# Kernel optimization log

Measured on AMD Instinct MI355X. Metric: run time of the kernel, lower is better.

Reference implementation:

```python
import jax, jax.numpy as jnp
import numpy as np

B, T, D, H, L = 64, 512, 1024, 1024, 2


def _make_params(key, in_size, hidden):
    # 4 input-to-hidden and 4 hidden-to-hidden matrices, gate order (i, f, n, o),
    # concatenated along the output axis -> one GEMM per source per step.
    k1, k2 = jax.random.split(key)
    sx = (6.0 / (in_size + hidden)) ** 0.5   # xavier_uniform bound
    sh = (6.0 / (hidden + hidden)) ** 0.5
    Wx = jax.random.uniform(k1, (in_size, 4 * hidden), minval=-sx, maxval=sx, dtype=jnp.float32)
    Wh = jax.random.uniform(k2, (hidden, 4 * hidden), minval=-sh, maxval=sh, dtype=jnp.float32)
    b = jnp.zeros((4 * hidden,), dtype=jnp.float32)
    return Wx, Wh, b


def setup_inputs() -> dict:
    key = jax.random.key(0)
    kx, k0, k1 = jax.random.split(key, 3)
    x = jax.random.normal(kx, (B, T, D), dtype=jnp.float32)
    h0 = jnp.zeros((L, B, H), dtype=jnp.float32)
    c0 = jnp.zeros((L, B, H), dtype=jnp.float32)
    Wx0, Wh0, b0 = _make_params(k0, D, H)
    Wx1, Wh1, b1 = _make_params(k1, H, H)
    return {"x": x, "h0": h0, "c0": c0,
            "Wx0": Wx0, "Wh0": Wh0, "b0": b0,
            "Wx1": Wx1, "Wh1": Wh1, "b1": b1}


def _run_layer(xseq, h, c, Wx, Wh, b):
    # xseq: [T, B, in], h/c: [B, H]
    def step(carry, xt):
        h, c = carry
        g = xt @ Wx + h @ Wh + b                       # [B, 4H]
        i_t, f_t, n_t, o_t = jnp.split(g, 4, axis=-1)
        i_t = jax.nn.sigmoid(i_t)
        f_t = jax.nn.sigmoid(f_t)
        n_t = jnp.tanh(n_t)
        o_t = jax.nn.sigmoid(o_t)
        c = f_t * c + i_t * n_t
        h = o_t * jnp.tanh(c)
        return (h, c), h
    (h, c), ys = jax.lax.scan(step, (h, c), xseq)
    return ys, h, c                                     # ys: [T, B, H]


def reference(x, h0, c0, Wx0, Wh0, b0, Wx1, Wh1, b1):
    xs = jnp.transpose(x, (1, 0, 2))                    # [T, B, D]
    params = [(Wx0, Wh0, b0), (Wx1, Wh1, b1)]
    hs, cs = [], []
    for layer in range(L):
        Wx, Wh, b = params[layer]
        xs, h, c = _run_layer(xs, h0[layer], c0[layer], Wx, Wh, b)
        hs.append(h)
        cs.append(c)
    outputs = jnp.transpose(xs, (1, 0, 2))              # [B, T, H]
    return outputs, (jnp.stack(hs, 0), jnp.stack(cs, 0))
```

## Files before the change

### kernel.cpp

```cpp
#include <hip/hip_runtime.h>


#define NBLK 256
#define TPB  512
#define T_   512
#define HS_OFF 33554432
#define CS_OFF 33685504

typedef float  f32x4  __attribute__((ext_vector_type(4)));
typedef short  bf16x8 __attribute__((ext_vector_type(8)));

#define WS_CTR  0u
#define WS_W    69632u
#define WS_BIAS 33624064u
#define WS_XB   33656832u
#define WS_H0   100765696u
#define WS_H1   101027840u
#define WS_MIN  101289984u
#define WS_XG   101289984u
#define WS_BIG  369725440u

__device__ __forceinline__ unsigned short f2bf(float f) {
  union { float f; unsigned u; } v; v.f = f;
  return (unsigned short)((v.u + 0x7FFFu + ((v.u >> 16) & 1u)) >> 16);
}
__device__ __forceinline__ float bf2f(unsigned short s) {
  union { unsigned u; float f; } v; v.u = ((unsigned)s) << 16;
  return v.f;
}
__device__ __forceinline__ float fsig(float x) { return 1.0f / (1.0f + __expf(-x)); }
__device__ __forceinline__ float ftanh(float x) {
  x = fminf(15.0f, fmaxf(-15.0f, x));
  float e = __expf(2.0f * x);
  return (e - 1.0f) / (e + 1.0f);
}

__global__ void kw(const float* __restrict__ Wx0, const float* __restrict__ Wh0,
                   const float* __restrict__ Wx1, const float* __restrict__ Wh1,
                   unsigned short* __restrict__ wp) {
  __shared__ float tile[64][65];
  int tb = blockIdx.x;
  int m  = tb >> 10;
  int kt = (tb >> 6) & 15;
  int nt = tb & 63;
  const float* W = (m == 0) ? Wx0 : (m == 1) ? Wh0 : (m == 2) ? Wx1 : Wh1;
  unsigned short* O = wp + (size_t)m * 4194304u;
  int k0 = kt * 64, n0 = nt * 64;
  int tx = threadIdx.x & 63, tg = threadIdx.x >> 6;
  for (int r = tg; r < 64; r += 4)
    tile[r][tx] = W[(size_t)(k0 + r) * 4096 + n0 + tx];
  __syncthreads();
  for (int r = tg; r < 64; r += 4) {
    int n = n0 + r;
    int p = ((n & 1023) << 2) | (n >> 10);
    O[(size_t)p * 1024 + k0 + tx] = f2bf(tile[tx][r]);
  }
}

__global__ void kx(const float* __restrict__ x, unsigned short* __restrict__ xb) {
  int row = blockIdx.x;
  int t = row >> 6, b = row & 63;
  const float4* src = (const float4*)(x + ((size_t)b * 512 + t) * 1024);
  float4 f = src[threadIdx.x];
  ushort4 o; o.x = f2bf(f.x); o.y = f2bf(f.y); o.z = f2bf(f.z); o.w = f2bf(f.w);
  ((ushort4*)(xb + (size_t)row * 1024))[threadIdx.x] = o;
}

__global__ void kmisc(const float* __restrict__ b0, const float* __restrict__ b1,
                      const float* __restrict__ h0in,
                      float* __restrict__ biasP,
                      unsigned short* __restrict__ h0r, unsigned short* __restrict__ h1r) {
  int idx = blockIdx.x * 256 + threadIdx.x;
  if (idx < 8192) {
    int layer = idx >> 12, p = idx & 4095;
    int orig = (p & 3) * 1024 + (p >> 2);
    biasP[idx] = (layer ? b1 : b0)[orig];
  } else if (idx < 139264) {
    int e = idx - 8192;
    int layer = e >> 16, o = e & 65535;
    int row = o >> 10, col = o & 1023;
    unsigned short v = f2bf(h0in[layer * 65536 + o]);
    int dst = 65536 + (col >> 3) * 512 + row * 8 + (col & 7);
    if (layer) h1r[dst] = v; else h0r[dst] = v;
  }
}

__global__ void __launch_bounds__(512, 2)
kxg(const unsigned short* __restrict__ wp, const unsigned short* __restrict__ xb,
    unsigned short* __restrict__ xg) {
  __shared__ char sm[73728];
  float* red = (float*)(sm + 65536);
  const int tid = threadIdx.x;
  const int w = tid >> 6, l = tid & 63;
  const int cb = blockIdx.x >> 4;
  const int tc = blockIdx.x & 15;
  const int rt = w & 3, kh = w >> 2;

  const char* src = (const char*)(wp + (size_t)(cb * 32) * 1024u);
  for (int i = tid; i < 4096; i += 512) {
    int sb = i << 4;
    int c  = sb >> 11;
    int kb = sb & 2047;
    *(uint4*)(sm + (c << 11) + (kb ^ ((c & 7) << 4))) = *(const uint4*)(src + sb);
  }
  __syncthreads();

  const int ae0 = (rt * 16 + (l & 15)) * 1024 + kh * 512 + (l >> 4) * 8;
  const int kb2 = kh * 1024 + (l >> 4) * 16;
  const int swz = (l & 7) << 4;
  const int lb0 = (l & 15) << 11;
  const int lb1 = ((l & 15) + 16) << 11;

  for (int t = tc * 32; t < tc * 32 + 32; ++t) {
    const unsigned short* xt = xb + (size_t)t * 65536u;
    f32x4 a0 = {0.f, 0.f, 0.f, 0.f};
    f32x4 a1 = {0.f, 0.f, 0.f, 0.f};
    #pragma unroll
    for (int kk = 0; kk < 16; ++kk) {
      bf16x8 ax = *(const bf16x8*)(xt + ae0 + kk * 32);
      const int kb = (kb2 + kk * 64) ^ swz;
      bf16x8 b0 = *(const bf16x8*)(sm + lb0 + kb);
      bf16x8 b1 = *(const bf16x8*)(sm + lb1 + kb);
      a0 = __builtin_amdgcn_mfma_f32_16x16x32_bf16(ax, b0, a0, 0, 0, 0);
      a1 = __builtin_amdgcn_mfma_f32_16x16x32_bf16(ax, b1, a1, 0, 0, 0);
    }
    if (kh == 1) {
      float* r0 = red + (size_t)((rt * 2 + 0) * 64 + l) * 4;
      float* r1 = red + (size_t)((rt * 2 + 1) * 64 + l) * 4;
      #pragma unroll
      for (int v = 0; v < 4; ++v) { r0[v] = a0[v]; r1[v] = a1[v]; }
    }
    __syncthreads();
    if (kh == 0) {
      const float* r0 = red + (size_t)((rt * 2 + 0) * 64 + l) * 4;
      const float* r1 = red + (size_t)((rt * 2 + 1) * 64 + l) * 4;
      ushort4 o0, o1;
      o0.x = f2bf(a0[0] + r0[0]); o0.y = f2bf(a0[1] + r0[1]);
      o0.z = f2bf(a0[2] + r0[2]); o0.w = f2bf(a0[3] + r0[3]);
      o1.x = f2bf(a1[0] + r1[0]); o1.y = f2bf(a1[1] + r1[1]);
      o1.z = f2bf(a1[2] + r1[2]); o1.w = f2bf(a1[3] + r1[3]);
      *(ushort4*)(xg + ((((size_t)t * 256 + (cb * 2 + 0)) * 4 + rt) * 64 + l) * 4) = o0;
      *(ushort4*)(xg + ((((size_t)t * 256 + (cb * 2 + 1)) * 4 + rt) * 64 + l) * 4) = o1;
    }
    __syncthreads();
  }
}

__global__ void __launch_bounds__(TPB)
klstm(const float* __restrict__ c0_in,
      const unsigned short* __restrict__ wp,
      const float* __restrict__ biasP,
      const unsigned short* __restrict__ xb,
      const unsigned short* __restrict__ xg,
      unsigned short* __restrict__ h0ring,
      unsigned short* __restrict__ h1ring,
      unsigned* __restrict__ ctrbase,
      float* __restrict__ out,
      int use_xg) {
  extern __shared__ char smem[];
  float* red = (float*)(smem + 131072);
  float* lhb = (float*)(smem + 139264);
  unsigned* gctr  = ctrbase;
  unsigned* rctr  = ctrbase + 8192;
  unsigned* gflag = ctrbase + 9216;
  const int tid = threadIdx.x;
  const int w   = tid >> 6;
  const int l   = tid & 63;
  const int bid = blockIdx.x;
  const int n0  = bid * 16;
  const int layer = w >> 2;
  const int rbase = (w & 3) * 16;
  const int khalf = (w >> 2) * 512;
  const int grp   = bid >> 5;
  float* lh = lhb + w * 64;

  for (int m = 0; m < 4; m += 2) {
    const char* src = (const char*)(wp + (size_t)m * 4194304u + (size_t)n0 * 1024u);
    char* dst = smem + m * 32768;
    for (int i = tid; i < 2048; i += TPB) {
      int sb = i << 4;
      int c  = sb >> 11;
      int kb = sb & 2047;
      *(uint4*)(dst + (c << 11) + (kb ^ ((c & 7) << 4))) = *(const uint4*)(src + sb);
    }
  }

  bf16x8 wh0f[16], wh1f[16];
  {
    const unsigned short* p0 = wp + 4194304u + (size_t)(n0 + (l & 15)) * 1024u + khalf + (l >> 4) * 8;
    const unsigned short* p1 = wp + 3u * 4194304u + (size_t)(n0 + (l & 15)) * 1024u + khalf + (l >> 4) * 8;
    #pragma unroll
    for (int ks = 0; ks < 16; ++ks) {
      wh0f[ks] = *(const bf16x8*)(p0 + ks * 32);
      wh1f[ks] = *(const bf16x8*)(p1 + ks * 32);
    }
  }

  const int jg = bid * 4 + ((l & 15) >> 2);
  const float biasv = biasP[layer * 4096 + n0 + (l & 15)];
  const int qb = l & ~3;

  float cr[4];
  #pragma unroll
  for (int v = 0; v < 4; ++v)
    cr[v] = c0_in[layer * 65536 + (rbase + (l >> 4) * 4 + v) * 1024 + jg];
  __syncthreads();

  const int ae0  = (rbase + (l & 15)) * 1024 + khalf + (l >> 4) * 8;
  const int hbase = ((khalf >> 3) + (l >> 4)) * 512 + (rbase + (l & 15)) * 8;
  const int lb0  = (l & 15) << 11;
  const int kb2  = khalf * 2 + (l >> 4) * 16;
  const int swz  = (l & 7) << 4;
  const int hsto = (bid >> 1) * 512 + 4 * (bid & 1);

  float xgf[4] = {0.f, 0.f, 0.f, 0.f};
  if (use_xg && w < 4) {
    ushort4 xv = *(const ushort4*)(xg + (((size_t)bid * 4 + w) * 64 + l) * 4);
    xgf[0] = bf2f(xv.x); xgf[1] = bf2f(xv.y); xgf[2] = bf2f(xv.z); xgf[3] = bf2f(xv.w);
  }

  for (int k = 0; k <= T_; ++k) {
    #pragma unroll
    for (int ks = 0; ks < 16; ++ks) {
      asm volatile("" :: "v"(wh0f[ks]));
      asm volatile("" :: "v"(wh1f[ks]));
    }

    const unsigned short* h0p = h0ring + ((k + 1) & 1) * 65536;
    const unsigned short* h1p = h1ring + (k & 1) * 65536;

    f32x4 acc0  = {0.f, 0.f, 0.f, 0.f};
    f32x4 acc0b = {0.f, 0.f, 0.f, 0.f};
    f32x4 acc1a = {0.f, 0.f, 0.f, 0.f};
    f32x4 acc1b = {0.f, 0.f, 0.f, 0.f};
    if (use_xg) {
      #pragma unroll
      for (int kk = 0; kk < 16; ++kk) {
        bf16x8 ah0 = *(const bf16x8*)(h0p + hbase + kk * 2048);
        bf16x8 ah1 = *(const bf16x8*)(h1p + hbase + kk * 2048);
        const int bo = lb0 + ((kb2 + kk * 64) ^ swz);
        bf16x8 bx1 = *(const bf16x8*)(smem + 65536 + bo);
        acc0  = __builtin_amdgcn_mfma_f32_16x16x32_bf16(ah0, wh0f[kk], acc0, 0, 0, 0);
        acc1a = __builtin_amdgcn_mfma_f32_16x16x32_bf16(ah0, bx1, acc1a, 0, 0, 0);
        acc1b = __builtin_amdgcn_mfma_f32_16x16x32_bf16(ah1, wh1f[kk], acc1b, 0, 0, 0);
      }
    } else {
      const unsigned short* xt = xb + (size_t)((k < T_) ? k : (T_ - 1)) * 65536u;
      #pragma unroll
      for (int kk = 0; kk < 16; ++kk) {
        bf16x8 ax  = *(const bf16x8*)(xt + ae0 + kk * 32);
        bf16x8 ah0 = *(const bf16x8*)(h0p + hbase + kk * 2048);
        bf16x8 ah1 = *(const bf16x8*)(h1p + hbase + kk * 2048);
        const int bo = lb0 + ((kb2 + kk * 64) ^ swz);
        bf16x8 bx0 = *(const bf16x8*)(smem + bo);
        bf16x8 bx1 = *(const bf16x8*)(smem + 65536 + bo);
        acc0b = __builtin_amdgcn_mfma_f32_16x16x32_bf16(ax,  bx0, acc0b, 0, 0, 0);
        acc0  = __builtin_amdgcn_mfma_f32_16x16x32_bf16(ah0, wh0f[kk], acc0, 0, 0, 0);
        acc1a = __builtin_amdgcn_mfma_f32_16x16x32_bf16(ah0, bx1, acc1a, 0, 0, 0);
        acc1b = __builtin_amdgcn_mfma_f32_16x16x32_bf16(ah1, wh1f[kk], acc1b, 0, 0, 0);
      }
    }

    {
      float* rb = red + (size_t)(w * 64 + l) * 4;
      f32x4 other = layer ? (acc0 + acc0b) : (acc1a + acc1b);
      #pragma unroll
      for (int v = 0; v < 4; ++v) rb[v] = other[v];
    }
    __syncthreads();

    f32x4 g = layer ? (acc1a + acc1b) : (acc0 + acc0b);
    {
      const int pw = layer ? (w - 4) : (w + 4);
      const float* rb = red + (size_t)(pw * 64 + l) * 4;
      #pragma unroll
      for (int v = 0; v < 4; ++v) g[v] += rb[v];
    }
    if (use_xg && w < 4) {
      #pragma unroll
      for (int v = 0; v < 4; ++v) g[v] += xgf[v];
    }

    const bool active = layer ? (k >= 1) : (k < T_);
    f32x4 outv = {0.f, 0.f, 0.f, 0.f};
    if (active) {
      unsigned short* hw = layer ? (h1ring + ((k + 1) & 1) * 65536)
                                 : (h0ring + (k & 1) * 65536);
      #pragma unroll
      for (int v = 0; v < 4; ++v) {
        float gv = g[v] + biasv;
        float gi = __shfl(gv, qb);
        float gf = __shfl(gv, qb | 1);
        float gn = __shfl(gv, qb | 2);
        float go = __shfl(gv, qb | 3);
        float i_ = fsig(gi), f_ = fsig(gf), n_ = ftanh(gn), o_ = fsig(go);
        float c = f_ * cr[v] + i_ * n_;
        cr[v] = c;
        float h = o_ * ftanh(c);
        if ((l & 3) == 0)
          lh[((l >> 4) * 4 + v) * 4 + ((l & 15) >> 2)] = h;
      }
      if (l < 16) {
        f32x4 h4 = *(f32x4*)(lh + l * 4);
        outv = h4;
        ushort4 u4;
        u4.x = f2bf(h4[0]); u4.y = f2bf(h4[1]); u4.z = f2bf(h4[2]); u4.w = f2bf(h4[3]);
        union { ushort4 s; unsigned long long q; } pk; pk.s = u4;
        __hip_atomic_store((unsigned long long*)(hw + hsto + (rbase + l) * 8), pk.q,
                           __ATOMIC_RELAXED, __HIP_MEMORY_SCOPE_AGENT);
      }
    }

    if (k < T_) {
      __syncthreads();
      if (tid == 0) {
        unsigned old = __hip_atomic_fetch_add(&gctr[grp * 1024 + k], 1u,
                                              __ATOMIC_RELAXED, __HIP_MEMORY_SCOPE_AGENT);
        if (old == 31u) {
          unsigned oldr = __hip_atomic_fetch_add(&rctr[k], 1u,
                                                 __ATOMIC_RELAXED, __HIP_MEMORY_SCOPE_AGENT);
          if (oldr == 7u) {
            #pragma unroll
            for (int gg = 0; gg < 8; ++gg)
              __hip_atomic_store(&gflag[gg * 1024 + k], 1u,
                                 __ATOMIC_RELAXED, __HIP_MEMORY_SCOPE_AGENT);
          }
        }
        __builtin_amdgcn_fence(__ATOMIC_ACQUIRE, "agent");
      }
    }

    if (active && l < 16) {
      const int row = rbase + l;
      if (layer) {
        *(f32x4*)(out + (size_t)row * 524288u + (size_t)(k - 1) * 1024u + bid * 4) = outv;
        if (k == T_)
          *(f32x4*)(out + HS_OFF + 65536 + row * 1024 + bid * 4) = outv;
      } else if (k == T_ - 1) {
        *(f32x4*)(out + HS_OFF + row * 1024 + bid * 4) = outv;
      }
    }
    if (use_xg && w < 4 && k + 1 < T_) {
      ushort4 xv = *(const ushort4*)(xg + ((((size_t)(k + 1) * 256 + bid) * 4 + w) * 64 + l) * 4);
      xgf[0] = bf2f(xv.x); xgf[1] = bf2f(xv.y); xgf[2] = bf2f(xv.z); xgf[3] = bf2f(xv.w);
    }

    if (k < T_) {
      if (tid == 0) {
        unsigned spins = 0;
        while (__hip_atomic_load(&gflag[grp * 1024 + k], __ATOMIC_RELAXED, __HIP_MEMORY_SCOPE_AGENT) == 0u) {
          __builtin_amdgcn_s_sleep(1);
          if (++spins > 67108864u) break;
        }
      }
      __syncthreads();
    }
  }

  if ((l & 3) == 0) {
    #pragma unroll
    for (int v = 0; v < 4; ++v)
      out[CS_OFF + layer * 65536 + (rbase + (l >> 4) * 4 + v) * 1024 + jg] = cr[v];
  }
}

extern "C" void kernel_launch(void* const* d_in, const int* in_sizes, int n_in,
                              void* d_out, int out_size, void* d_ws, size_t ws_size,
                              hipStream_t stream) {
  const float* x   = (const float*)d_in[0];
  const float* h0  = (const float*)d_in[1];
  const float* c0  = (const float*)d_in[2];
  const float* Wx0 = (const float*)d_in[3];
  const float* Wh0 = (const float*)d_in[4];
  const float* b0  = (const float*)d_in[5];
  const float* Wx1 = (const float*)d_in[6];
  const float* Wh1 = (const float*)d_in[7];
  const float* b1  = (const float*)d_in[8];
  float* out = (float*)d_out;
  char* ws = (char*)d_ws;
  if (ws_size < (size_t)WS_MIN) return;
  const int use_xg = (ws_size >= (size_t)WS_BIG) ? 1 : 0;

  unsigned* ctr       = (unsigned*)(ws + WS_CTR);
  unsigned short* wp  = (unsigned short*)(ws + WS_W);
  float* biasP        = (float*)(ws + WS_BIAS);
  unsigned short* xbp = (unsigned short*)(ws + WS_XB);
  unsigned short* h0r = (unsigned short*)(ws + WS_H0);
  unsigned short* h1r = (unsigned short*)(ws + WS_H1);
  unsigned short* xgp = (unsigned short*)(ws + WS_XG);

  (void)hipMemsetAsync(ctr, 0, 69632, stream);
  hipLaunchKernelGGL(kw,    dim3(4096),  dim3(256), 0, stream, Wx0, Wh0, Wx1, Wh1, wp);
  hipLaunchKernelGGL(kx,    dim3(32768), dim3(256), 0, stream, x, xbp);
  hipLaunchKernelGGL(kmisc, dim3(544),   dim3(256), 0, stream, b0, b1, h0, biasP, h0r, h1r);
  if (use_xg)
    hipLaunchKernelGGL(kxg, dim3(2048),  dim3(512), 0, stream, wp, xbp, xgp);

  (void)hipFuncSetAttribute((const void*)klstm, hipFuncAttributeMaxDynamicSharedMemorySize, 141312);
  const float* c0a = c0; const unsigned short* wpa = wp; const float* bpa = biasP;
  const unsigned short* xba = xbp; const unsigned short* xga = xgp;
  unsigned short* h0a = h0r; unsigned short* h1a = h1r;
  unsigned* ca = ctr; float* oa = out; int uxg = use_xg;
  void* args[] = {&c0a, &wpa, &bpa, &xba, &xga, &h0a, &h1a, &ca, &oa, &uxg};
  hipError_t e = hipLaunchCooperativeKernel((const void*)klstm, dim3(NBLK), dim3(TPB),
                                            args, 141312, stream);
  if (e != hipSuccess) {
    hipLaunchKernelGGL(klstm, dim3(NBLK), dim3(TPB), 141312, stream,
                       c0a, wpa, bpa, xba, xga, h0a, h1a, ca, oa, uxg);
  }
}
```

Baseline: 5.768 ms.

## Double threads per block and split K across wave pairs per layer

```diff
diff --git a/kernel.cpp b/kernel.cpp
--- a/kernel.cpp
+++ b/kernel.cpp
@@ -2,7 +2,7 @@
 
 
 #define NBLK 256
-#define TPB  512
+#define TPB  1024
 #define T_   512
 #define HS_OFF 33554432
 #define CS_OFF 33685504
@@ -158,8 +158,8 @@
       float* __restrict__ out,
       int use_xg) {
   extern __shared__ char smem[];
-  float* red = (float*)(smem + 131072);
-  float* lhb = (float*)(smem + 139264);
+  float* red = (float*)(smem + 65536);
+  float* lhb = (float*)(smem + 73728);
   unsigned* gctr  = ctrbase;
   unsigned* rctr  = ctrbase + 8192;
   unsigned* gflag = ctrbase + 9216;
@@ -168,42 +168,52 @@
   const int l   = tid & 63;
   const int bid = blockIdx.x;
   const int n0  = bid * 16;
-  const int layer = w >> 2;
-  const int rbase = (w & 3) * 16;
-  const int khalf = (w >> 2) * 512;
+  const int lay = w >> 3;
+  const int rt  = (w >> 1) & 3;
+  const int kh  = w & 1;
+  const int rbase = rt * 16;
+  const int khalf = kh * 512;
   const int grp   = bid >> 5;
-  float* lh = lhb + w * 64;
-
-  for (int m = 0; m < 4; m += 2) {
-    const char* src = (const char*)(wp + (size_t)m * 4194304u + (size_t)n0 * 1024u);
-    char* dst = smem + m * 32768;
+  const int slot  = lay * 4 + rt;
+  float* lh = lhb + slot * 64;
+
+  {
+    const char* src = (const char*)(wp + 2u * 4194304u + (size_t)n0 * 1024u);
     for (int i = tid; i < 2048; i += TPB) {
       int sb = i << 4;
       int c  = sb >> 11;
       int kb = sb & 2047;
-      *(uint4*)(dst + (c << 11) + (kb ^ ((c & 7) << 4))) = *(const uint4*)(src + sb);
-    }
-  }
-
-  bf16x8 wh0f[16], wh1f[16];
+      *(uint4*)(smem + (c << 11) + (kb ^ ((c & 7) << 4))) = *(const uint4*)(src + sb);
+    }
+    if (!use_xg) {
+      const char* s0 = (const char*)(wp + (size_t)n0 * 1024u);
+      for (int i = tid; i < 2048; i += TPB) {
+        int sb = i << 4;
+        int c  = sb >> 11;
+        int kb = sb & 2047;
+        *(uint4*)(smem + 32768 + (c << 11) + (kb ^ ((c & 7) << 4))) = *(const uint4*)(s0 + sb);
+      }
+    }
+  }
+
+  bf16x8 whf[16];
   {
-    const unsigned short* p0 = wp + 4194304u + (size_t)(n0 + (l & 15)) * 1024u + khalf + (l >> 4) * 8;
-    const unsigned short* p1 = wp + 3u * 4194304u + (size_t)(n0 + (l & 15)) * 1024u + khalf + (l >> 4) * 8;
+    const unsigned short* pw_ = wp + (size_t)(lay ? 3u : 1u) * 4194304u
+                              + (size_t)(n0 + (l & 15)) * 1024u + khalf + (l >> 4) * 8;
     #pragma unroll
-    for (int ks = 0; ks < 16; ++ks) {
-      wh0f[ks] = *(const bf16x8*)(p0 + ks * 32);
-      wh1f[ks] = *(const bf16x8*)(p1 + ks * 32);
-    }
+    for (int ks = 0; ks < 16; ++ks) whf[ks] = *(const bf16x8*)(pw_ + ks * 32);
   }
 
   const int jg = bid * 4 + ((l & 15) >> 2);
-  const float biasv = biasP[layer * 4096 + n0 + (l & 15)];
+  const float biasv = biasP[lay * 4096 + n0 + (l & 15)];
   const int qb = l & ~3;
 
-  float cr[4];
-  #pragma unroll
-  for (int v = 0; v < 4; ++v)
-    cr[v] = c0_in[layer * 65536 + (rbase + (l >> 4) * 4 + v) * 1024 + jg];
+  float cr[4] = {0.f, 0.f, 0.f, 0.f};
+  if (kh == 0) {
+    #pragma unroll
+    for (int v = 0; v < 4; ++v)
+      cr[v] = c0_in[lay * 65536 + (rbase + (l >> 4) * 4 + v) * 1024 + jg];
+  }
   __syncthreads();
 
   const int ae0  = (rbase + (l & 15)) * 1024 + khalf + (l >> 4) * 8;
@@ -214,78 +224,69 @@
   const int hsto = (bid >> 1) * 512 + 4 * (bid & 1);
 
   float xgf[4] = {0.f, 0.f, 0.f, 0.f};
-  if (use_xg && w < 4) {
-    ushort4 xv = *(const ushort4*)(xg + (((size_t)bid * 4 + w) * 64 + l) * 4);
+  if (use_xg && lay == 0 && kh == 0) {
+    ushort4 xv = *(const ushort4*)(xg + (((size_t)bid * 4 + rt) * 64 + l) * 4);
     xgf[0] = bf2f(xv.x); xgf[1] = bf2f(xv.y); xgf[2] = bf2f(xv.z); xgf[3] = bf2f(xv.w);
   }
 
   for (int k = 0; k <= T_; ++k) {
     #pragma unroll
-    for (int ks = 0; ks < 16; ++ks) {
-      asm volatile("" :: "v"(wh0f[ks]));
-      asm volatile("" :: "v"(wh1f[ks]));
-    }
+    for (int ks = 0; ks < 16; ++ks) asm volatile("" :: "v"(whf[ks]));
 
     const unsigned short* h0p = h0ring + ((k + 1) & 1) * 65536;
     const unsigned short* h1p = h1ring + (k & 1) * 65536;
 
-    f32x4 acc0  = {0.f, 0.f, 0.f, 0.f};
-    f32x4 acc0b = {0.f, 0.f, 0.f, 0.f};
-    f32x4 acc1a = {0.f, 0.f, 0.f, 0.f};
-    f32x4 acc1b = {0.f, 0.f, 0.f, 0.f};
-    if (use_xg) {
+    f32x4 accA = {0.f, 0.f, 0.f, 0.f};
+    f32x4 accB = {0.f, 0.f, 0.f, 0.f};
+    if (lay == 0) {
+      #pragma unroll
+      for (int kk = 0; kk < 16; ++kk) {
+        bf16x8 ah0 = *(const bf16x8*)(h0p + hbase + kk * 2048);
+        accA = __builtin_amdgcn_mfma_f32_16x16x32_bf16(ah0, whf[kk], accA, 0, 0, 0);
+      }
+      if (!use_xg) {
+        const unsigned short* xt = xb + (size_t)((k < T_) ? k : (T_ - 1)) * 65536u;
+        #pragma unroll
+        for (int kk = 0; kk < 16; ++kk) {
+          bf16x8 ax  = *(const bf16x8*)(xt + ae0 + kk * 32);
+          bf16x8 bx0 = *(const bf16x8*)(smem + 32768 + lb0 + ((kb2 + kk * 64) ^ swz));
+          accB = __builtin_amdgcn_mfma_f32_16x16x32_bf16(ax, bx0, accB, 0, 0, 0);
+        }
+      }
+    } else {
       #pragma unroll
       for (int kk = 0; kk < 16; ++kk) {
         bf16x8 ah0 = *(const bf16x8*)(h0p + hbase + kk * 2048);
         bf16x8 ah1 = *(const bf16x8*)(h1p + hbase + kk * 2048);
-        const int bo = lb0 + ((kb2 + kk * 64) ^ swz);
-        bf16x8 bx1 = *(const bf16x8*)(smem + 65536 + bo);
-        acc0  = __builtin_amdgcn_mfma_f32_16x16x32_bf16(ah0, wh0f[kk], acc0, 0, 0, 0);
-        acc1a = __builtin_amdgcn_mfma_f32_16x16x32_bf16(ah0, bx1, acc1a, 0, 0, 0);
-        acc1b = __builtin_amdgcn_mfma_f32_16x16x32_bf16(ah1, wh1f[kk], acc1b, 0, 0, 0);
-      }
-    } else {
-      const unsigned short* xt = xb + (size_t)((k < T_) ? k : (T_ - 1)) * 65536u;
+        bf16x8 bx1 = *(const bf16x8*)(smem + lb0 + ((kb2 + kk * 64) ^ swz));
+        accA = __builtin_amdgcn_mfma_f32_16x16x32_bf16(ah0, bx1, accA, 0, 0, 0);
+        accB = __builtin_amdgcn_mfma_f32_16x16x32_bf16(ah1, whf[kk], accB, 0, 0, 0);
+      }
+    }
+
+    if (kh == 1) {
+      float* rb = red + (size_t)slot * 256 + (size_t)l * 4;
+      f32x4 s = accA + accB;
       #pragma unroll
-      for (int kk = 0; kk < 16; ++kk) {
-        bf16x8 ax  = *(const bf16x8*)(xt + ae0 + kk * 32);
-        bf16x8 ah0 = *(const bf16x8*)(h0p + hbase + kk * 2048);
-        bf16x8 ah1 = *(const bf16x8*)(h1p + hbase + kk * 2048);
-        const int bo = lb0 + ((kb2 + kk * 64) ^ swz);
-        bf16x8 bx0 = *(const bf16x8*)(smem + bo);
-        bf16x8 bx1 = *(const bf16x8*)(smem + 65536 + bo);
-        acc0b = __builtin_amdgcn_mfma_f32_16x16x32_bf16(ax,  bx0, acc0b, 0, 0, 0);
-        acc0  = __builtin_amdgcn_mfma_f32_16x16x32_bf16(ah0, wh0f[kk], acc0, 0, 0, 0);
-        acc1a = __builtin_amdgcn_mfma_f32_16x16x32_bf16(ah0, bx1, acc1a, 0, 0, 0);
-        acc1b = __builtin_amdgcn_mfma_f32_16x16x32_bf16(ah1, wh1f[kk], acc1b, 0, 0, 0);
-      }
-    }
-
-    {
-      float* rb = red + (size_t)(w * 64 + l) * 4;
-      f32x4 other = layer ? (acc0 + acc0b) : (acc1a + acc1b);
-      #pragma unroll
-      for (int v = 0; v < 4; ++v) rb[v] = other[v];
+      for (int v = 0; v < 4; ++v) rb[v] = s[v];
     }
     __syncthreads();
 
-    f32x4 g = layer ? (acc1a + acc1b) : (acc0 + acc0b);
-    {
-      const int pw = layer ? (w - 4) : (w + 4);
-      const float* rb = red + (size_t)(pw * 64 + l) * 4;
-      #pragma unroll
-      for (int v = 0; v < 4; ++v) g[v] += rb[v];
-    }
-    if (use_xg && w < 4) {
-      #pragma unroll
-      for (int v = 0; v < 4; ++v) g[v] += xgf[v];
-    }
-
-    const bool active = layer ? (k >= 1) : (k < T_);
+    const bool active = lay ? (k >= 1) : (k < T_);
     f32x4 outv = {0.f, 0.f, 0.f, 0.f};
-    if (active) {
-      unsigned short* hw = layer ? (h1ring + ((k + 1) & 1) * 65536)
-                                 : (h0ring + (k & 1) * 65536);
+    if (kh == 0 && active) {
+      f32x4 g = accA + accB;
+      {
+        const float* rb = red + (size_t)slot * 256 + (size_t)l * 4;
+        #pragma unroll
+        for (int v = 0; v < 4; ++v) g[v] += rb[v];
+      }
+      if (lay == 0) {
+        #pragma unroll
+        for (int v = 0; v < 4; ++v) g[v] += xgf[v];
+      }
+      unsigned short* hw = lay ? (h1ring + ((k + 1) & 1) * 65536)
+                               : (h0ring + (k & 1) * 65536);
       #pragma unroll
       for (int v = 0; v < 4; ++v) {
         float gv = g[v] + biasv;
@@ -330,9 +331,9 @@
       }
     }
 
-    if (active && l < 16) {
+    if (kh == 0 && active && l < 16) {
       const int row = rbase + l;
-      if (layer) {
+      if (lay) {
         *(f32x4*)(out + (size_t)row * 524288u + (size_t)(k - 1) * 1024u + bid * 4) = outv;
         if (k == T_)
           *(f32x4*)(out + HS_OFF + 65536 + row * 1024 + bid * 4) = outv;
@@ -340,8 +341,8 @@
         *(f32x4*)(out + HS_OFF + row * 1024 + bid * 4) = outv;
       }
     }
-    if (use_xg && w < 4 && k + 1 < T_) {
-      ushort4 xv = *(const ushort4*)(xg + ((((size_t)(k + 1) * 256 + bid) * 4 + w) * 64 + l) * 4);
+    if (use_xg && lay == 0 && kh == 0 && k + 1 < T_) {
+      ushort4 xv = *(const ushort4*)(xg + ((((size_t)(k + 1) * 256 + bid) * 4 + rt) * 64 + l) * 4);
       xgf[0] = bf2f(xv.x); xgf[1] = bf2f(xv.y); xgf[2] = bf2f(xv.z); xgf[3] = bf2f(xv.w);
     }
 
@@ -357,10 +358,10 @@
     }
   }
 
-  if ((l & 3) == 0) {
+  if (kh == 0 && (l & 3) == 0) {
     #pragma unroll
     for (int v = 0; v < 4; ++v)
-      out[CS_OFF + layer * 65536 + (rbase + (l >> 4) * 4 + v) * 1024 + jg] = cr[v];
+      out[CS_OFF + lay * 65536 + (rbase + (l >> 4) * 4 + v) * 1024 + jg] = cr[v];
   }
 }
 
@@ -396,16 +397,16 @@
   if (use_xg)
     hipLaunchKernelGGL(kxg, dim3(2048),  dim3(512), 0, stream, wp, xbp, xgp);
 
-  (void)hipFuncSetAttribute((const void*)klstm, hipFuncAttributeMaxDynamicSharedMemorySize, 141312);
+  (void)hipFuncSetAttribute((const void*)klstm, hipFuncAttributeMaxDynamicSharedMemorySize, 75776);
   const float* c0a = c0; const unsigned short* wpa = wp; const float* bpa = biasP;
   const unsigned short* xba = xbp; const unsigned short* xga = xgp;
   unsigned short* h0a = h0r; unsigned short* h1a = h1r;
   unsigned* ca = ctr; float* oa = out; int uxg = use_xg;
   void* args[] = {&c0a, &wpa, &bpa, &xba, &xga, &h0a, &h1a, &ca, &oa, &uxg};
   hipError_t e = hipLaunchCooperativeKernel((const void*)klstm, dim3(NBLK), dim3(TPB),
-                                            args, 141312, stream);
+                                            args, 75776, stream);
   if (e != hipSuccess) {
-    hipLaunchKernelGGL(klstm, dim3(NBLK), dim3(TPB), 141312, stream,
+    hipLaunchKernelGGL(klstm, dim3(NBLK), dim3(TPB), 75776, stream,
                        c0a, wpa, bpa, xba, xga, h0a, h1a, ca, oa, uxg);
   }
 }
```

Result: slower. 6.571 ms (+13.9%).

## Drop precomputed x-projection kernel; compute next-step layer-0 input GEMM inside recurrent loop

Applied to the files above, without the earlier changes.

```diff
diff --git a/kernel.cpp b/kernel.cpp
--- a/kernel.cpp
+++ b/kernel.cpp
@@ -17,16 +17,10 @@
 #define WS_H0   100765696u
 #define WS_H1   101027840u
 #define WS_MIN  101289984u
-#define WS_XG   101289984u
-#define WS_BIG  369725440u
 
 __device__ __forceinline__ unsigned short f2bf(float f) {
   union { float f; unsigned u; } v; v.f = f;
   return (unsigned short)((v.u + 0x7FFFu + ((v.u >> 16) & 1u)) >> 16);
-}
-__device__ __forceinline__ float bf2f(unsigned short s) {
-  union { unsigned u; float f; } v; v.u = ((unsigned)s) << 16;
-  return v.f;
 }
 __device__ __forceinline__ float fsig(float x) { return 1.0f / (1.0f + __expf(-x)); }
 __device__ __forceinline__ float ftanh(float x) {
@@ -85,81 +79,19 @@
   }
 }
 
-__global__ void __launch_bounds__(512, 2)
-kxg(const unsigned short* __restrict__ wp, const unsigned short* __restrict__ xb,
-    unsigned short* __restrict__ xg) {
-  __shared__ char sm[73728];
-  float* red = (float*)(sm + 65536);
-  const int tid = threadIdx.x;
-  const int w = tid >> 6, l = tid & 63;
-  const int cb = blockIdx.x >> 4;
-  const int tc = blockIdx.x & 15;
-  const int rt = w & 3, kh = w >> 2;
-
-  const char* src = (const char*)(wp + (size_t)(cb * 32) * 1024u);
-  for (int i = tid; i < 4096; i += 512) {
-    int sb = i << 4;
-    int c  = sb >> 11;
-    int kb = sb & 2047;
-    *(uint4*)(sm + (c << 11) + (kb ^ ((c & 7) << 4))) = *(const uint4*)(src + sb);
-  }
-  __syncthreads();
-
-  const int ae0 = (rt * 16 + (l & 15)) * 1024 + kh * 512 + (l >> 4) * 8;
-  const int kb2 = kh * 1024 + (l >> 4) * 16;
-  const int swz = (l & 7) << 4;
-  const int lb0 = (l & 15) << 11;
-  const int lb1 = ((l & 15) + 16) << 11;
-
-  for (int t = tc * 32; t < tc * 32 + 32; ++t) {
-    const unsigned short* xt = xb + (size_t)t * 65536u;
-    f32x4 a0 = {0.f, 0.f, 0.f, 0.f};
-    f32x4 a1 = {0.f, 0.f, 0.f, 0.f};
-    #pragma unroll
-    for (int kk = 0; kk < 16; ++kk) {
-      bf16x8 ax = *(const bf16x8*)(xt + ae0 + kk * 32);
-      const int kb = (kb2 + kk * 64) ^ swz;
-      bf16x8 b0 = *(const bf16x8*)(sm + lb0 + kb);
-      bf16x8 b1 = *(const bf16x8*)(sm + lb1 + kb);
-      a0 = __builtin_amdgcn_mfma_f32_16x16x32_bf16(ax, b0, a0, 0, 0, 0);
-      a1 = __builtin_amdgcn_mfma_f32_16x16x32_bf16(ax, b1, a1, 0, 0, 0);
-    }
-    if (kh == 1) {
-      float* r0 = red + (size_t)((rt * 2 + 0) * 64 + l) * 4;
-      float* r1 = red + (size_t)((rt * 2 + 1) * 64 + l) * 4;
-      #pragma unroll
-      for (int v = 0; v < 4; ++v) { r0[v] = a0[v]; r1[v] = a1[v]; }
-    }
-    __syncthreads();
-    if (kh == 0) {
-      const float* r0 = red + (size_t)((rt * 2 + 0) * 64 + l) * 4;
-      const float* r1 = red + (size_t)((rt * 2 + 1) * 64 + l) * 4;
-      ushort4 o0, o1;
-      o0.x = f2bf(a0[0] + r0[0]); o0.y = f2bf(a0[1] + r0[1]);
-      o0.z = f2bf(a0[2] + r0[2]); o0.w = f2bf(a0[3] + r0[3]);
-      o1.x = f2bf(a1[0] + r1[0]); o1.y = f2bf(a1[1] + r1[1]);
-      o1.z = f2bf(a1[2] + r1[2]); o1.w = f2bf(a1[3] + r1[3]);
-      *(ushort4*)(xg + ((((size_t)t * 256 + (cb * 2 + 0)) * 4 + rt) * 64 + l) * 4) = o0;
-      *(ushort4*)(xg + ((((size_t)t * 256 + (cb * 2 + 1)) * 4 + rt) * 64 + l) * 4) = o1;
-    }
-    __syncthreads();
-  }
-}
-
 __global__ void __launch_bounds__(TPB)
 klstm(const float* __restrict__ c0_in,
       const unsigned short* __restrict__ wp,
       const float* __restrict__ biasP,
       const unsigned short* __restrict__ xb,
-      const unsigned short* __restrict__ xg,
       unsigned short* __restrict__ h0ring,
       unsigned short* __restrict__ h1ring,
       unsigned* __restrict__ ctrbase,
-      float* __restrict__ out,
-      int use_xg) {
+      float* __restrict__ out) {
   extern __shared__ char smem[];
-  float* red = (float*)(smem + 131072);
-  float* lhb = (float*)(smem + 139264);
+  float* red  = (float*)(smem + 65536);
+  float* lhb  = (float*)(smem + 73728);
+  float* xred = (float*)(smem + 75776);
   unsigned* gctr  = ctrbase;
   unsigned* rctr  = ctrbase + 8192;
   unsigned* gflag = ctrbase + 9216;
@@ -176,7 +108,7 @@
 
   for (int m = 0; m < 4; m += 2) {
     const char* src = (const char*)(wp + (size_t)m * 4194304u + (size_t)n0 * 1024u);
-    char* dst = smem + m * 32768;
+    char* dst = smem + (m >> 1) * 32768;
     for (int i = tid; i < 2048; i += TPB) {
       int sb = i << 4;
       int c  = sb >> 11;
@@ -204,7 +136,6 @@
   #pragma unroll
   for (int v = 0; v < 4; ++v)
     cr[v] = c0_in[layer * 65536 + (rbase + (l >> 4) * 4 + v) * 1024 + jg];
-  __syncthreads();
 
   const int ae0  = (rbase + (l & 15)) * 1024 + khalf + (l >> 4) * 8;
   const int hbase = ((khalf >> 3) + (l >> 4)) * 512 + (rbase + (l & 15)) * 8;
@@ -213,11 +144,23 @@
   const int swz  = (l & 7) << 4;
   const int hsto = (bid >> 1) * 512 + 4 * (bid & 1);
 
-  float xgf[4] = {0.f, 0.f, 0.f, 0.f};
-  if (use_xg && w < 4) {
-    ushort4 xv = *(const ushort4*)(xg + (((size_t)bid * 4 + w) * 64 + l) * 4);
-    xgf[0] = bf2f(xv.x); xgf[1] = bf2f(xv.y); xgf[2] = bf2f(xv.z); xgf[3] = bf2f(xv.w);
-  }
+  __syncthreads();
+
+  f32x4 xacc = {0.f, 0.f, 0.f, 0.f};
+  {
+    #pragma unroll
+    for (int kk = 0; kk < 16; ++kk) {
+      bf16x8 ax = *(const bf16x8*)(xb + ae0 + kk * 32);
+      bf16x8 b  = *(const bf16x8*)(smem + lb0 + ((kb2 + kk * 64) ^ swz));
+      xacc = __builtin_amdgcn_mfma_f32_16x16x32_bf16(ax, b, xacc, 0, 0, 0);
+    }
+    if (w >= 4) {
+      float* xr = xred + (size_t)(w & 3) * 256 + (size_t)l * 4;
+      #pragma unroll
+      for (int v = 0; v < 4; ++v) xr[v] = xacc[v];
+    }
+  }
+  __syncthreads();
 
   for (int k = 0; k <= T_; ++k) {
     #pragma unroll
@@ -230,55 +173,37 @@
     const unsigned short* h1p = h1ring + (k & 1) * 65536;
 
     f32x4 acc0  = {0.f, 0.f, 0.f, 0.f};
-    f32x4 acc0b = {0.f, 0.f, 0.f, 0.f};
     f32x4 acc1a = {0.f, 0.f, 0.f, 0.f};
     f32x4 acc1b = {0.f, 0.f, 0.f, 0.f};
-    if (use_xg) {
-      #pragma unroll
-      for (int kk = 0; kk < 16; ++kk) {
-        bf16x8 ah0 = *(const bf16x8*)(h0p + hbase + kk * 2048);
-        bf16x8 ah1 = *(const bf16x8*)(h1p + hbase + kk * 2048);
-        const int bo = lb0 + ((kb2 + kk * 64) ^ swz);
-        bf16x8 bx1 = *(const bf16x8*)(smem + 65536 + bo);
-        acc0  = __builtin_amdgcn_mfma_f32_16x16x32_bf16(ah0, wh0f[kk], acc0, 0, 0, 0);
-        acc1a = __builtin_amdgcn_mfma_f32_16x16x32_bf16(ah0, bx1, acc1a, 0, 0, 0);
-        acc1b = __builtin_amdgcn_mfma_f32_16x16x32_bf16(ah1, wh1f[kk], acc1b, 0, 0, 0);
-      }
-    } else {
-      const unsigned short* xt = xb + (size_t)((k < T_) ? k : (T_ - 1)) * 65536u;
-      #pragma unroll
-      for (int kk = 0; kk < 16; ++kk) {
-        bf16x8 ax  = *(const bf16x8*)(xt + ae0 + kk * 32);
-        bf16x8 ah0 = *(const bf16x8*)(h0p + hbase + kk * 2048);
-        bf16x8 ah1 = *(const bf16x8*)(h1p + hbase + kk * 2048);
-        const int bo = lb0 + ((kb2 + kk * 64) ^ swz);
-        bf16x8 bx0 = *(const bf16x8*)(smem + bo);
-        bf16x8 bx1 = *(const bf16x8*)(smem + 65536 + bo);
-        acc0b = __builtin_amdgcn_mfma_f32_16x16x32_bf16(ax,  bx0, acc0b, 0, 0, 0);
-        acc0  = __builtin_amdgcn_mfma_f32_16x16x32_bf16(ah0, wh0f[kk], acc0, 0, 0, 0);
-        acc1a = __builtin_amdgcn_mfma_f32_16x16x32_bf16(ah0, bx1, acc1a, 0, 0, 0);
-        acc1b = __builtin_amdgcn_mfma_f32_16x16x32_bf16(ah1, wh1f[kk], acc1b, 0, 0, 0);
-      }
+    #pragma unroll
+    for (int kk = 0; kk < 16; ++kk) {
+      bf16x8 ah0 = *(const bf16x8*)(h0p + hbase + kk * 2048);
+      bf16x8 ah1 = *(const bf16x8*)(h1p + hbase + kk * 2048);
+      bf16x8 bx1 = *(const bf16x8*)(smem + 32768 + lb0 + ((kb2 + kk * 64) ^ swz));
+      acc0  = __builtin_amdgcn_mfma_f32_16x16x32_bf16(ah0, wh0f[kk], acc0, 0, 0, 0);
+      acc1a = __builtin_amdgcn_mfma_f32_16x16x32_bf16(ah0, bx1, acc1a, 0, 0, 0);
+      acc1b = __builtin_amdgcn_mfma_f32_16x16x32_bf16(ah1, wh1f[kk], acc1b, 0, 0, 0);
     }
 
     {
       float* rb = red + (size_t)(w * 64 + l) * 4;
-      f32x4 other = layer ? (acc0 + acc0b) : (acc1a + acc1b);
+      f32x4 other = layer ? acc0 : (acc1a + acc1b);
       #pragma unroll
       for (int v = 0; v < 4; ++v) rb[v] = other[v];
     }
     __syncthreads();
 
-    f32x4 g = layer ? (acc1a + acc1b) : (acc0 + acc0b);
+    f32x4 g = layer ? (acc1a + acc1b) : acc0;
     {
       const int pw = layer ? (w - 4) : (w + 4);
       const float* rb = red + (size_t)(pw * 64 + l) * 4;
       #pragma unroll
       for (int v = 0; v < 4; ++v) g[v] += rb[v];
     }
-    if (use_xg && w < 4) {
-      #pragma unroll
-      for (int v = 0; v < 4; ++v) g[v] += xgf[v];
+    if (w < 4) {
+      const float* xr = xred + (size_t)w * 256 + (size_t)l * 4;
+      #pragma unroll
+      for (int v = 0; v < 4; ++v) g[v] += xacc[v] + xr[v];
     }
 
     const bool active = layer ? (k >= 1) : (k < T_);
@@ -340,9 +265,22 @@
         *(f32x4*)(out + HS_OFF + row * 1024 + bid * 4) = outv;
       }
     }
-    if (use_xg && w < 4 && k + 1 < T_) {
-      ushort4 xv = *(const ushort4*)(xg + ((((size_t)(k + 1) * 256 + bid) * 4 + w) * 64 + l) * 4);
-      xgf[0] = bf2f(xv.x); xgf[1] = bf2f(xv.y); xgf[2] = bf2f(xv.z); xgf[3] = bf2f(xv.w);
+    if (k + 1 < T_) {
+      const unsigned short* xt = xb + (size_t)(k + 1) * 65536u;
+      f32x4 xa = {0.f, 0.f, 0.f, 0.f};
+      #pragma unroll
+      for (int kk = 0; kk < 16; ++kk) {
+        bf16x8 ax = *(const bf16x8*)(xt + ae0 + kk * 32);
+        bf16x8 b  = *(const bf16x8*)(smem + lb0 + ((kb2 + kk * 64) ^ swz));
+        xa = __builtin_amdgcn_mfma_f32_16x16x32_bf16(ax, b, xa, 0, 0, 0);
+      }
+      if (w >= 4) {
+        float* xr = xred + (size_t)(w & 3) * 256 + (size_t)l * 4;
+        #pragma unroll
+        for (int v = 0; v < 4; ++v) xr[v] = xa[v];
+      } else {
+        xacc = xa;
+      }
     }
 
     if (k < T_) {
@@ -379,7 +317,6 @@
   float* out = (float*)d_out;
   char* ws = (char*)d_ws;
   if (ws_size < (size_t)WS_MIN) return;
-  const int use_xg = (ws_size >= (size_t)WS_BIG) ? 1 : 0;
 
   unsigned* ctr       = (unsigned*)(ws + WS_CTR);
   unsigned short* wp  = (unsigned short*)(ws + WS_W);
@@ -387,25 +324,22 @@
   unsigned short* xbp = (unsigned short*)(ws + WS_XB);
   unsigned short* h0r = (unsigned short*)(ws + WS_H0);
   unsigned short* h1r = (unsigned short*)(ws + WS_H1);
-  unsigned short* xgp = (unsigned short*)(ws + WS_XG);
 
   (void)hipMemsetAsync(ctr, 0, 69632, stream);
   hipLaunchKernelGGL(kw,    dim3(4096),  dim3(256), 0, stream, Wx0, Wh0, Wx1, Wh1, wp);
   hipLaunchKernelGGL(kx,    dim3(32768), dim3(256), 0, stream, x, xbp);
   hipLaunchKernelGGL(kmisc, dim3(544),   dim3(256), 0, stream, b0, b1, h0, biasP, h0r, h1r);
-  if (use_xg)
-    hipLaunchKernelGGL(kxg, dim3(2048),  dim3(512), 0, stream, wp, xbp, xgp);
-
-  (void)hipFuncSetAttribute((const void*)klstm, hipFuncAttributeMaxDynamicSharedMemorySize, 141312);
+
+  (void)hipFuncSetAttribute((const void*)klstm, hipFuncAttributeMaxDynamicSharedMemorySize, 79872);
   const float* c0a = c0; const unsigned short* wpa = wp; const float* bpa = biasP;
-  const unsigned short* xba = xbp; const unsigned short* xga = xgp;
+  const unsigned short* xba = xbp;
   unsigned short* h0a = h0r; unsigned short* h1a = h1r;
-  unsigned* ca = ctr; float* oa = out; int uxg = use_xg;
-  void* args[] = {&c0a, &wpa, &bpa, &xba, &xga, &h0a, &h1a, &ca, &oa, &uxg};
+  unsigned* ca = ctr; float* oa = out;
+  void* args[] = {&c0a, &wpa, &bpa, &xba, &h0a, &h1a, &ca, &oa};
   hipError_t e = hipLaunchCooperativeKernel((const void*)klstm, dim3(NBLK), dim3(TPB),
-                                            args, 141312, stream);
+                                            args, 79872, stream);
   if (e != hipSuccess) {
-    hipLaunchKernelGGL(klstm, dim3(NBLK), dim3(TPB), 141312, stream,
-                       c0a, wpa, bpa, xba, xga, h0a, h1a, ca, oa, uxg);
-  }
-}
+    hipLaunchKernelGGL(klstm, dim3(NBLK), dim3(TPB), 79872, stream,
+                       c0a, wpa, bpa, xba, h0a, h1a, ca, oa);
+  }
+}
```

After: 5.623 ms. 2.5% less time.
